# Kernel tuning notes

Hardware: AMD Instinct MI355X
Metric: run time of the kernel (lower is better)

Reference implementation:

```python
import jax, jax.numpy as jnp
import numpy as np

B, H, L, D = 4, 16, 8192, 64


def setup_inputs() -> dict:
    key = jax.random.key(0)
    ks = jax.random.split(key, 10)
    q = jax.random.normal(ks[0], (B, H, L, D), dtype=jnp.float32)
    k = jax.random.normal(ks[1], (B, H, L, D), dtype=jnp.float32)
    v = jax.random.normal(ks[2], (B, H, L, D), dtype=jnp.float32)
    mask = jax.random.randint(ks[3], (B, H, L), 0, 2, dtype=jnp.int32)
    s = 1.0 / np.sqrt(D)
    Wa_w = jax.random.uniform(ks[4], (D, D), jnp.float32, -s, s)  # torch Linear weight [out,in]
    Wa_b = jax.random.uniform(ks[5], (D,), jnp.float32, -s, s)
    Ua_w = jax.random.uniform(ks[6], (D, D), jnp.float32, -s, s)
    Ua_b = jax.random.uniform(ks[7], (D,), jnp.float32, -s, s)
    va_w = jax.random.uniform(ks[8], (1, D), jnp.float32, -s, s)
    va_b = jax.random.uniform(ks[9], (1,), jnp.float32, -s, s)
    return {"q": q, "k": k, "v": v, "mask": mask,
            "Wa_w": Wa_w, "Wa_b": Wa_b, "Ua_w": Ua_w, "Ua_b": Ua_b,
            "va_w": va_w, "va_b": va_b}


def reference(q, k, v, mask, Wa_w, Wa_b, Ua_w, Ua_b, va_w, va_b):
    # e1 = Wa(q), e2 = Ua(k)  (torch Linear: x @ W.T + b)
    e1 = jnp.einsum('bhld,ed->bhle', q, Wa_w) + Wa_b
    e2 = jnp.einsum('bhld,ed->bhle', k, Ua_w) + Ua_b
    t = jnp.tanh(e1 + e2)
    # va: [B,H,L,D] -> [B,H,L]
    e = jnp.einsum('bhld,d->bhl', t, va_w[0]) + va_b[0]
    e = jnp.where(mask == 0, jnp.float32(-10000.0), e)
    alpha = jax.nn.softmax(e, axis=-1)  # softmax over sequence length
    return alpha[..., None] * v
```

## Files before the change

kernel.cpp:

```cpp
#include <hip/hip_runtime.h>
#include <hip/hip_bf16.h>

#define BH   64
#define LSEQ 8192
#define DDIM 64
#define NPOS (BH * LSEQ)
#define NT4  (NPOS * DDIM / 4)
#define TPB  16

typedef __attribute__((ext_vector_type(8))) short bf16x8;
typedef __attribute__((ext_vector_type(4))) float f32x4;

__device__ inline short f2bf(float f) {
    __bf16 b = (__bf16)f;
    return __builtin_bit_cast(short, b);
}
__device__ inline float bf2f(short s) {
    unsigned u = ((unsigned)(unsigned short)s) << 16;
    return __builtin_bit_cast(float, u);
}
__device__ inline void split8(const float* f, bf16x8& hi, bf16x8& lo) {
#pragma unroll
    for (int j = 0; j < 8; j++) {
        short h = f2bf(f[j]);
        hi[j] = h;
        lo[j] = f2bf(f[j] - bf2f(h));
    }
}
__device__ inline float tanh_fast(float x) {
    float ex = __expf(2.f * x);
    return 1.f - 2.f * __builtin_amdgcn_rcpf(ex + 1.f);
}

__global__ __launch_bounds__(64, 2) void score_kernel(
    const float* __restrict__ q, const float* __restrict__ k,
    const float* __restrict__ Waw, const float* __restrict__ Wab,
    const float* __restrict__ Uaw, const float* __restrict__ Uab,
    const float* __restrict__ vaw, const float* __restrict__ vab_p,
    float* __restrict__ e_out)
{
    const int lane = threadIdx.x;
    const int m    = lane & 15;
    const int g    = lane >> 4;
    const long t0  = (long)blockIdx.x * TPB;

    __shared__ float lds[2][2048];

    bf16x8 bwa[4][2], bua[4][2];
    float bias_s[4], vav[4];
#pragma unroll
    for (int t = 0; t < 4; t++) {
        const int n = t * 16 + m;
        bias_s[t] = Wab[n] + Uab[n];
        vav[t]    = vaw[n];
#pragma unroll
        for (int s = 0; s < 2; s++) {
            const int k0 = s * 32 + g * 8;
            const float4 wA = ((const float4*)(Waw + n * 64 + k0))[0];
            const float4 wB = ((const float4*)(Waw + n * 64 + k0))[1];
            const float4 uA = ((const float4*)(Uaw + n * 64 + k0))[0];
            const float4 uB = ((const float4*)(Uaw + n * 64 + k0))[1];
            float wf[8] = {wA.x, wA.y, wA.z, wA.w, wB.x, wB.y, wB.z, wB.w};
            float uf[8] = {uA.x, uA.y, uA.z, uA.w, uB.x, uB.y, uB.z, uB.w};
            bf16x8 wv, uv;
#pragma unroll
            for (int j = 0; j < 8; j++) { wv[j] = f2bf(wf[j]); uv[j] = f2bf(uf[j]); }
            bwa[t][s] = wv;
            bua[t][s] = uv;
        }
    }
    const float vab = vab_p[0];

    auto issue_tile = [&](long tile, int buf) {
        const float* qb = q + tile * 1024;
        const float* kb = k + tile * 1024;
#pragma unroll
        for (int i = 0; i < 4; i++) {
            const int row = 4 * i + g;
            const int c   = m ^ (row & 7);
            __builtin_amdgcn_global_load_lds(
                (const __attribute__((address_space(1))) void*)(qb + row * 64 + c * 4),
                (__attribute__((address_space(3))) void*)(&lds[buf][i * 256]),
                16, 0, 0);
            __builtin_amdgcn_global_load_lds(
                (const __attribute__((address_space(1))) void*)(kb + row * 64 + c * 4),
                (__attribute__((address_space(3))) void*)(&lds[buf][1024 + i * 256]),
                16, 0, 0);
        }
    };

    auto compute = [&](int buf, long tile) {
        f32x4 acc[4];
#pragma unroll
        for (int t = 0; t < 4; t++) acc[t] = (f32x4){0.f, 0.f, 0.f, 0.f};
        const float* L = lds[buf];
#pragma unroll
        for (int s = 0; s < 2; s++) {
            const int c0 = s * 8 + g * 2;
            const float4 qa = *((const float4*)(L + m * 64 + (( c0      ^ (m & 7)) << 2)));
            const float4 qb = *((const float4*)(L + m * 64 + (((c0 + 1) ^ (m & 7)) << 2)));
            const float4 ka = *((const float4*)(L + 1024 + m * 64 + (( c0      ^ (m & 7)) << 2)));
            const float4 kb = *((const float4*)(L + 1024 + m * 64 + (((c0 + 1) ^ (m & 7)) << 2)));
            float qf[8] = {qa.x, qa.y, qa.z, qa.w, qb.x, qb.y, qb.z, qb.w};
            float kf[8] = {ka.x, ka.y, ka.z, ka.w, kb.x, kb.y, kb.z, kb.w};
            bf16x8 qhi, qlo, khi, klo;
            split8(qf, qhi, qlo);
            split8(kf, khi, klo);
#pragma unroll
            for (int t = 0; t < 4; t++) {
                acc[t] = __builtin_amdgcn_mfma_f32_16x16x32_bf16(qhi, bwa[t][s], acc[t], 0, 0, 0);
                acc[t] = __builtin_amdgcn_mfma_f32_16x16x32_bf16(qlo, bwa[t][s], acc[t], 0, 0, 0);
                acc[t] = __builtin_amdgcn_mfma_f32_16x16x32_bf16(khi, bua[t][s], acc[t], 0, 0, 0);
                acc[t] = __builtin_amdgcn_mfma_f32_16x16x32_bf16(klo, bua[t][s], acc[t], 0, 0, 0);
            }
        }
        float c[4] = {0.f, 0.f, 0.f, 0.f};
#pragma unroll
        for (int t = 0; t < 4; t++) {
#pragma unroll
            for (int r = 0; r < 4; r++)
                c[r] += vav[t] * tanh_fast(acc[t][r] + bias_s[t]);
        }
#pragma unroll
        for (int r = 0; r < 4; r++) {
#pragma unroll
            for (int off2 = 1; off2 < 16; off2 <<= 1)
                c[r] += __shfl_xor(c[r], off2, 16);
        }
        if (m == 0) {
            float4 ev;
            ev.x = c[0] + vab;
            ev.y = c[1] + vab;
            ev.z = c[2] + vab;
            ev.w = c[3] + vab;
            *((float4*)(e_out + tile * 16 + g * 4)) = ev;
        }
    };

    asm volatile("s_waitcnt vmcnt(0)" ::: "memory");
    __builtin_amdgcn_sched_barrier(0);

    issue_tile(t0 + 0, 0);
    issue_tile(t0 + 1, 1);
    asm volatile("s_waitcnt vmcnt(8)" ::: "memory");
    __builtin_amdgcn_sched_barrier(0);
#pragma unroll 1
    for (int j = 0; j < TPB / 2 - 1; ++j) {
        const long tb = t0 + 2 * j;
        compute(0, tb + 0);
        issue_tile(tb + 2, 0);
        asm volatile("s_waitcnt vmcnt(9)" ::: "memory");
        __builtin_amdgcn_sched_barrier(0);
        compute(1, tb + 1);
        issue_tile(tb + 3, 1);
        asm volatile("s_waitcnt vmcnt(9)" ::: "memory");
        __builtin_amdgcn_sched_barrier(0);
    }
    compute(0, t0 + TPB - 2);
    asm volatile("s_waitcnt vmcnt(1)" ::: "memory");
    __builtin_amdgcn_sched_barrier(0);
    compute(1, t0 + TPB - 1);
}

__global__ __launch_bounds__(1024) void rowstat_kernel(
    const float* __restrict__ e, const int* __restrict__ mask,
    float* __restrict__ stats)
{
    const int row = blockIdx.x;
    const size_t base = (size_t)row * LSEQ;
    const int tid  = threadIdx.x;
    const int lane = tid & 63;
    const int wv   = tid >> 6;
    __shared__ float redmax[16];
    __shared__ float redsum[16];

    float4 e0 = ((const float4*)(e + base))[tid];
    float4 e1 = ((const float4*)(e + base))[1024 + tid];
    int4   m0 = ((const int4*)(mask + base))[tid];
    int4   m1 = ((const int4*)(mask + base))[1024 + tid];
    float em[8] = {m0.x ? e0.x : -10000.f, m0.y ? e0.y : -10000.f,
                   m0.z ? e0.z : -10000.f, m0.w ? e0.w : -10000.f,
                   m1.x ? e1.x : -10000.f, m1.y ? e1.y : -10000.f,
                   m1.z ? e1.z : -10000.f, m1.w ? e1.w : -10000.f};

    float lm = em[0];
#pragma unroll
    for (int j = 1; j < 8; j++) lm = fmaxf(lm, em[j]);
#pragma unroll
    for (int off = 32; off >= 1; off >>= 1) lm = fmaxf(lm, __shfl_xor(lm, off, 64));
    if (lane == 0) redmax[wv] = lm;
    __syncthreads();
    float M = redmax[0];
#pragma unroll
    for (int i = 1; i < 16; i++) M = fmaxf(M, redmax[i]);

    float ls = 0.f;
#pragma unroll
    for (int j = 0; j < 8; j++) ls += __expf(em[j] - M);
#pragma unroll
    for (int off = 32; off >= 1; off >>= 1) ls += __shfl_xor(ls, off, 64);
    if (lane == 0) redsum[wv] = ls;
    __syncthreads();
    if (tid == 0) {
        float S = 0.f;
#pragma unroll
        for (int i = 0; i < 16; i++) S += redsum[i];
        stats[row * 2]     = M;
        stats[row * 2 + 1] = 1.f / S;
    }
}

__global__ __launch_bounds__(256) void scale_kernel(
    const float* __restrict__ v, const float* __restrict__ e,
    const int* __restrict__ mask,
    const float* __restrict__ stats, float* __restrict__ out)
{
    const size_t b0 = (size_t)blockIdx.x * 1024 + threadIdx.x;
    const f32x4* vp = (const f32x4*)v;
    f32x4*       op = (f32x4*)out;

    size_t idx[4];
    f32x4  vv[4];
    float  ee[4];
    int    mm[4];
    float2 st[4];
#pragma unroll
    for (int j = 0; j < 4; j++) {
        idx[j] = b0 + (size_t)j * 256;
        vv[j]  = __builtin_nontemporal_load(vp + idx[j]);
    }
#pragma unroll
    for (int j = 0; j < 4; j++) {
        const size_t p = idx[j] >> 4;
        ee[j] = e[p];
        mm[j] = mask[p];
        st[j] = ((const float2*)stats)[p >> 13];
    }
#pragma unroll
    for (int j = 0; j < 4; j++) {
        const float a = mm[j] ? __expf(ee[j] - st[j].x) * st[j].y : 0.f;
        f32x4 o = vv[j] * a;
        __builtin_nontemporal_store(o, op + idx[j]);
    }
}

extern "C" void kernel_launch(void* const* d_in, const int* in_sizes, int n_in,
                              void* d_out, int out_size, void* d_ws, size_t ws_size,
                              hipStream_t stream) {
    const float* q    = (const float*)d_in[0];
    const float* k    = (const float*)d_in[1];
    const float* v    = (const float*)d_in[2];
    const int*   mask = (const int*)d_in[3];
    const float* Waw  = (const float*)d_in[4];
    const float* Wab  = (const float*)d_in[5];
    const float* Uaw  = (const float*)d_in[6];
    const float* Uab  = (const float*)d_in[7];
    const float* vaw  = (const float*)d_in[8];
    const float* vab  = (const float*)d_in[9];
    float* out = (float*)d_out;

    float* e_buf = (float*)d_ws;
    float* stats = (float*)d_ws + NPOS;

    score_kernel<<<NPOS / (16 * TPB), 64, 0, stream>>>(q, k, Waw, Wab, Uaw, Uab, vaw, vab, e_buf);
    rowstat_kernel<<<BH, 1024, 0, stream>>>(e_buf, mask, stats);
    scale_kernel<<<NT4 / 1024, 256, 0, stream>>>(v, e_buf, mask, stats, out);
}
```

Before: 418.6 us.

## Replace persistent LDS-pipelined score kernel with one-tile-per-block direct loads

```diff
diff --git a/kernel.cpp b/kernel.cpp
--- a/kernel.cpp
+++ b/kernel.cpp
@@ -6,7 +6,6 @@
 #define DDIM 64
 #define NPOS (BH * LSEQ)
 #define NT4  (NPOS * DDIM / 4)
-#define TPB  16
 
 typedef __attribute__((ext_vector_type(8))) short bf16x8;
 typedef __attribute__((ext_vector_type(4))) float f32x4;
@@ -32,7 +31,7 @@
     return 1.f - 2.f * __builtin_amdgcn_rcpf(ex + 1.f);
 }
 
-__global__ __launch_bounds__(64, 2) void score_kernel(
+__global__ __launch_bounds__(64) void score_kernel(
     const float* __restrict__ q, const float* __restrict__ k,
     const float* __restrict__ Waw, const float* __restrict__ Wab,
     const float* __restrict__ Uaw, const float* __restrict__ Uab,
@@ -41,10 +40,18 @@
 {
     const int lane = threadIdx.x;
     const int m    = lane & 15;
-    const int g    = lane >> 4;
-    const long t0  = (long)blockIdx.x * TPB;
-
-    __shared__ float lds[2][2048];
+    const int quad = lane >> 4;
+    const long tile = blockIdx.x;
+
+    const size_t off = (size_t)(tile * 16 + m) * 64 + quad * 8;
+    const float4 b0 = *((const float4*)(q + off));
+    const float4 b1 = *((const float4*)(q + off + 4));
+    const float4 b2 = *((const float4*)(k + off));
+    const float4 b3 = *((const float4*)(k + off + 4));
+    const float4 b4 = *((const float4*)(q + off + 32));
+    const float4 b5 = *((const float4*)(q + off + 36));
+    const float4 b6 = *((const float4*)(k + off + 32));
+    const float4 b7 = *((const float4*)(k + off + 36));
 
     bf16x8 bwa[4][2], bua[4][2];
     float bias_s[4], vav[4];
@@ -55,7 +62,7 @@
         vav[t]    = vaw[n];
 #pragma unroll
         for (int s = 0; s < 2; s++) {
-            const int k0 = s * 32 + g * 8;
+            const int k0 = s * 32 + quad * 8;
             const float4 wA = ((const float4*)(Waw + n * 64 + k0))[0];
             const float4 wB = ((const float4*)(Waw + n * 64 + k0))[1];
             const float4 uA = ((const float4*)(Uaw + n * 64 + k0))[0];
@@ -71,95 +78,47 @@
     }
     const float vab = vab_p[0];
 
-    auto issue_tile = [&](long tile, int buf) {
-        const float* qb = q + tile * 1024;
-        const float* kb = k + tile * 1024;
-#pragma unroll
-        for (int i = 0; i < 4; i++) {
-            const int row = 4 * i + g;
-            const int c   = m ^ (row & 7);
-            __builtin_amdgcn_global_load_lds(
-                (const __attribute__((address_space(1))) void*)(qb + row * 64 + c * 4),
-                (__attribute__((address_space(3))) void*)(&lds[buf][i * 256]),
-                16, 0, 0);
-            __builtin_amdgcn_global_load_lds(
-                (const __attribute__((address_space(1))) void*)(kb + row * 64 + c * 4),
-                (__attribute__((address_space(3))) void*)(&lds[buf][1024 + i * 256]),
-                16, 0, 0);
+    f32x4 acc[4];
+#pragma unroll
+    for (int t = 0; t < 4; t++) acc[t] = (f32x4){0.f, 0.f, 0.f, 0.f};
+#pragma unroll
+    for (int s = 0; s < 2; s++) {
+        const float4 qa = s ? b4 : b0, qb = s ? b5 : b1;
+        const float4 ka = s ? b6 : b2, kb = s ? b7 : b3;
+        float qf[8] = {qa.x, qa.y, qa.z, qa.w, qb.x, qb.y, qb.z, qb.w};
+        float kf[8] = {ka.x, ka.y, ka.z, ka.w, kb.x, kb.y, kb.z, kb.w};
+        bf16x8 qhi, qlo, khi, klo;
+        split8(qf, qhi, qlo);
+        split8(kf, khi, klo);
+#pragma unroll
+        for (int t = 0; t < 4; t++) {
+            acc[t] = __builtin_amdgcn_mfma_f32_16x16x32_bf16(qhi, bwa[t][s], acc[t], 0, 0, 0);
+            acc[t] = __builtin_amdgcn_mfma_f32_16x16x32_bf16(qlo, bwa[t][s], acc[t], 0, 0, 0);
+            acc[t] = __builtin_amdgcn_mfma_f32_16x16x32_bf16(khi, bua[t][s], acc[t], 0, 0, 0);
+            acc[t] = __builtin_amdgcn_mfma_f32_16x16x32_bf16(klo, bua[t][s], acc[t], 0, 0, 0);
         }
-    };
-
-    auto compute = [&](int buf, long tile) {
-        f32x4 acc[4];
-#pragma unroll
-        for (int t = 0; t < 4; t++) acc[t] = (f32x4){0.f, 0.f, 0.f, 0.f};
-        const float* L = lds[buf];
-#pragma unroll
-        for (int s = 0; s < 2; s++) {
-            const int c0 = s * 8 + g * 2;
-            const float4 qa = *((const float4*)(L + m * 64 + (( c0      ^ (m & 7)) << 2)));
-            const float4 qb = *((const float4*)(L + m * 64 + (((c0 + 1) ^ (m & 7)) << 2)));
-            const float4 ka = *((const float4*)(L + 1024 + m * 64 + (( c0      ^ (m & 7)) << 2)));
-            const float4 kb = *((const float4*)(L + 1024 + m * 64 + (((c0 + 1) ^ (m & 7)) << 2)));
-            float qf[8] = {qa.x, qa.y, qa.z, qa.w, qb.x, qb.y, qb.z, qb.w};
-            float kf[8] = {ka.x, ka.y, ka.z, ka.w, kb.x, kb.y, kb.z, kb.w};
-            bf16x8 qhi, qlo, khi, klo;
-            split8(qf, qhi, qlo);
-            split8(kf, khi, klo);
-#pragma unroll
-            for (int t = 0; t < 4; t++) {
-                acc[t] = __builtin_amdgcn_mfma_f32_16x16x32_bf16(qhi, bwa[t][s], acc[t], 0, 0, 0);
-                acc[t] = __builtin_amdgcn_mfma_f32_16x16x32_bf16(qlo, bwa[t][s], acc[t], 0, 0, 0);
-                acc[t] = __builtin_amdgcn_mfma_f32_16x16x32_bf16(khi, bua[t][s], acc[t], 0, 0, 0);
-                acc[t] = __builtin_amdgcn_mfma_f32_16x16x32_bf16(klo, bua[t][s], acc[t], 0, 0, 0);
-            }
-        }
-        float c[4] = {0.f, 0.f, 0.f, 0.f};
-#pragma unroll
-        for (int t = 0; t < 4; t++) {
-#pragma unroll
-            for (int r = 0; r < 4; r++)
-                c[r] += vav[t] * tanh_fast(acc[t][r] + bias_s[t]);
-        }
-#pragma unroll
-        for (int r = 0; r < 4; r++) {
-#pragma unroll
-            for (int off2 = 1; off2 < 16; off2 <<= 1)
-                c[r] += __shfl_xor(c[r], off2, 16);
-        }
-        if (m == 0) {
-            float4 ev;
-            ev.x = c[0] + vab;
-            ev.y = c[1] + vab;
-            ev.z = c[2] + vab;
-            ev.w = c[3] + vab;
-            *((float4*)(e_out + tile * 16 + g * 4)) = ev;
-        }
-    };
-
-    asm volatile("s_waitcnt vmcnt(0)" ::: "memory");
-    __builtin_amdgcn_sched_barrier(0);
-
-    issue_tile(t0 + 0, 0);
-    issue_tile(t0 + 1, 1);
-    asm volatile("s_waitcnt vmcnt(8)" ::: "memory");
-    __builtin_amdgcn_sched_barrier(0);
-#pragma unroll 1
-    for (int j = 0; j < TPB / 2 - 1; ++j) {
-        const long tb = t0 + 2 * j;
-        compute(0, tb + 0);
-        issue_tile(tb + 2, 0);
-        asm volatile("s_waitcnt vmcnt(9)" ::: "memory");
-        __builtin_amdgcn_sched_barrier(0);
-        compute(1, tb + 1);
-        issue_tile(tb + 3, 1);
-        asm volatile("s_waitcnt vmcnt(9)" ::: "memory");
-        __builtin_amdgcn_sched_barrier(0);
-    }
-    compute(0, t0 + TPB - 2);
-    asm volatile("s_waitcnt vmcnt(1)" ::: "memory");
-    __builtin_amdgcn_sched_barrier(0);
-    compute(1, t0 + TPB - 1);
+    }
+    float c[4] = {0.f, 0.f, 0.f, 0.f};
+#pragma unroll
+    for (int t = 0; t < 4; t++) {
+#pragma unroll
+        for (int r = 0; r < 4; r++)
+            c[r] += vav[t] * tanh_fast(acc[t][r] + bias_s[t]);
+    }
+#pragma unroll
+    for (int r = 0; r < 4; r++) {
+#pragma unroll
+        for (int off2 = 1; off2 < 16; off2 <<= 1)
+            c[r] += __shfl_xor(c[r], off2, 16);
+    }
+    if (m == 0) {
+        float4 ev;
+        ev.x = c[0] + vab;
+        ev.y = c[1] + vab;
+        ev.z = c[2] + vab;
+        ev.w = c[3] + vab;
+        *((float4*)(e_out + tile * 16 + quad * 4)) = ev;
+    }
 }
 
 __global__ __launch_bounds__(1024) void rowstat_kernel(
@@ -262,7 +221,7 @@
     float* e_buf = (float*)d_ws;
     float* stats = (float*)d_ws + NPOS;
 
-    score_kernel<<<NPOS / (16 * TPB), 64, 0, stream>>>(q, k, Waw, Wab, Uaw, Uab, vaw, vab, e_buf);
+    score_kernel<<<NPOS / 16, 64, 0, stream>>>(q, k, Waw, Wab, Uaw, Uab, vaw, vab, e_buf);
     rowstat_kernel<<<BH, 1024, 0, stream>>>(e_buf, mask, stats);
     scale_kernel<<<NT4 / 1024, 256, 0, stream>>>(v, e_buf, mask, stats, out);
 }
```

Measured after the change: 458.2 us. 9.5% more time.
